# Optimization experiments

Hardware: AMD Instinct MI355X
Metric: run time of the kernel (lower is better)

## Reference

```python
import jax, jax.numpy as jnp
import numpy as np

QMIN, QMAX = 0.0, 255.0  # uint8 activation quantization range


def _qlinear(x, w_q, b, s_in, zp_in, s_w):
    """zentorch_qlinear: quantize fp32 x to uint8, int8 weight, dequant output.

    x:   [M, K] fp32
    w_q: [N, K] int8 values (stored int32), symmetric (weight zp = 0)
    b:   [N] fp32
    s_in, zp_in: scalars (activation scale / zero point)
    s_w: [N] per-output-channel weight scales
    """
    zp = zp_in.astype(jnp.float32)
    q = jnp.clip(jnp.round(x / s_in) + zp, QMIN, QMAX)      # fake-quant uint8
    x_dq = (q - zp) * s_in                                   # dequantized activation
    w_dq = w_q.astype(jnp.float32) * s_w[:, None]            # [N, K] dequant weight
    return x_dq @ w_dq.T + b                                 # [M, N] fp32


def setup_inputs() -> dict:
    key = jax.random.key(0)
    k1, k2, k3, k4 = jax.random.split(key, 4)
    M, K, N = 8192, 4096, 4096
    inp = {
        "input": jax.random.normal(k1, (M, K), dtype=jnp.float32),
        "weights": jax.random.randint(k2, (N, K), -128, 128, dtype=jnp.int32),
        "biases": jax.random.normal(k3, (N,), dtype=jnp.float32) * 0.1,
        "input_scales": jnp.array([0.05], dtype=jnp.float32),
        "input_zero_points": jnp.array([128], dtype=jnp.int32),
        "weight_scales": jax.random.uniform(k4, (N,), dtype=jnp.float32, minval=0.001, maxval=0.01),
        "weight_zero_points": jnp.zeros((N,), dtype=jnp.int32),
        "output_dtype": 0,  # 0 -> float32
    }
    return inp


def reference(input, weights, biases, input_scales, input_zero_points,
              weight_scales, weight_zero_points, output_dtype):
    s_in = input_scales[0]
    zp_in = input_zero_points[0]
    x = _qlinear(input, weights, biases, s_in, zp_in, weight_scales)
    x = _qlinear(x, weights, biases, s_in, zp_in, weight_scales)
    x = _qlinear(x, weights, biases, s_in, zp_in, weight_scales)
    return x
```

## Files before the change

kernel.cpp:

```cpp
#include <hip/hip_runtime.h>
#include <stdint.h>

#define M_DIM 8192
#define K_DIM 4096
#define N_DIM 4096
#define KTILES (K_DIM / 64)

typedef __attribute__((ext_vector_type(4))) int i32x4;

__global__ void pack_w_kernel(const int* __restrict__ w, char* __restrict__ wp,
                              int* __restrict__ corr, const int* __restrict__ zpp) {
  __shared__ int red[256];
  const int n = blockIdx.x;
  const int t = threadIdx.x;
  const int kt = t >> 2;
  const int g = t & 3;
  const int* row = w + (size_t)n * K_DIM + kt * 64 + g * 16;
  int s = 0;
  int words[4];
#pragma unroll
  for (int u = 0; u < 4; ++u) {
    int4 v = *(const int4*)(row + u * 4);
    s += v.x + v.y + v.z + v.w;
    words[u] = (v.x & 255) | ((v.y & 255) << 8) | ((v.z & 255) << 16) | (v.w << 24);
  }
  const int b = n & ~63;
  const int idx = n & 63;
  const int j = idx & 3;
  const int r = idx >> 2;
  const int F = (b >> 4) + j;
  char* dst = wp + ((size_t)F * 64 + kt) * 1024 + (g * 16 + r) * 16;
  *(int4*)dst = make_int4(words[0], words[1], words[2], words[3]);
  red[t] = s;
  __syncthreads();
  for (int off = 128; off > 0; off >>= 1) {
    if (t < off) red[t] += red[t + off];
    __syncthreads();
  }
  if (t == 0) corr[n] = (128 - zpp[0]) * red[0];
}

__global__ void quant_in_kernel(const float* __restrict__ x, char* __restrict__ q,
                                const float* __restrict__ sp, const int* __restrict__ zpp) {
  const int i = blockIdx.x * blockDim.x + threadIdx.x;
  const float s = sp[0];
  const float zp = (float)zpp[0];
  float4 v = ((const float4*)x)[i];
  float t0 = fminf(fmaxf(rintf(v.x / s) + zp, 0.f), 255.f);
  float t1 = fminf(fmaxf(rintf(v.y / s) + zp, 0.f), 255.f);
  float t2 = fminf(fmaxf(rintf(v.z / s) + zp, 0.f), 255.f);
  float t3 = fminf(fmaxf(rintf(v.w / s) + zp, 0.f), 255.f);
  int b0 = (int)t0 - 128, b1 = (int)t1 - 128, b2 = (int)t2 - 128, b3 = (int)t3 - 128;
  ((int*)q)[i] = (b0 & 255) | ((b1 & 255) << 8) | ((b2 & 255) << 16) | (b3 << 24);
}

#define STAGE16(SRC, DST)                                                     \
  __builtin_amdgcn_global_load_lds(                                           \
      (const __attribute__((address_space(1))) void*)(SRC),                   \
      (__attribute__((address_space(3))) void*)(DST), 16, 0, 0)

#define RD(p) (*(const i32x4*)(p))

#define TILE(SLOT, KSTG, TN, DO_NEXT)                                         \
  {                                                                           \
    const char* bufA_ = &lds[SLOT][0];                                        \
    char* nA_ = &lds[((SLOT) + 3) & 3][0];                                    \
    i32x4 a1_[4];                                                             \
    _Pragma("unroll") for (int i_ = 0; i_ < 4; ++i_)                          \
        a1_[i_] = RD(bufA_ + aoff[4 + i_]);                                   \
    STAGE16(asrc0 + (size_t)(KSTG) * 64, nA_ + o0_);                          \
    STAGE16(asrc1 + (size_t)(KSTG) * 64, nA_ + o1_);                          \
    __builtin_amdgcn_s_setprio(1);                                            \
    _Pragma("unroll") for (int i_ = 0; i_ < 4; ++i_)                          \
        _Pragma("unroll") for (int j_ = 0; j_ < 4; ++j_)                      \
            acc[i_][j_] = __builtin_amdgcn_mfma_i32_16x16x64_i8(              \
                a0[i_], b0[j_], acc[i_][j_], 0, 0, 0);                        \
    __builtin_amdgcn_s_setprio(0);                                            \
    i32x4 ta_[4], bn_[4];                                                     \
    if (DO_NEXT) {                                                            \
      const char* xA_ = &lds[((SLOT) + 1) & 3][0];                            \
      _Pragma("unroll") for (int i_ = 0; i_ < 4; ++i_)                        \
          ta_[i_] = RD(xA_ + aoff[i_]);                                       \
      _Pragma("unroll") for (int j_ = 0; j_ < 4; ++j_)                        \
          bn_[j_] = RD(bptr[j_] + (size_t)(TN) * 1024);                       \
    }                                                                         \
    __builtin_amdgcn_s_setprio(1);                                            \
    _Pragma("unroll") for (int i_ = 0; i_ < 4; ++i_)                          \
        _Pragma("unroll") for (int j_ = 0; j_ < 4; ++j_)                      \
            acc[4 + i_][j_] = __builtin_amdgcn_mfma_i32_16x16x64_i8(          \
                a1_[i_], b0[j_], acc[4 + i_][j_], 0, 0, 0);                   \
    __builtin_amdgcn_s_setprio(0);                                            \
    asm volatile("s_waitcnt vmcnt(12)" ::: "memory");                         \
    __builtin_amdgcn_s_barrier();                                             \
    if (DO_NEXT) {                                                            \
      _Pragma("unroll") for (int i_ = 0; i_ < 4; ++i_) a0[i_] = ta_[i_];      \
      _Pragma("unroll") for (int j_ = 0; j_ < 4; ++j_) b0[j_] = bn_[j_];      \
    }                                                                         \
  }

template <int WRITE_Q>
__global__ __launch_bounds__(512, 2) void gemm_kernel(
    const char* __restrict__ qa, const char* __restrict__ wbp,
    const int* __restrict__ corr, const float* __restrict__ swp,
    const float* __restrict__ bias, const float* __restrict__ sp,
    const int* __restrict__ zpp, char* __restrict__ outq, float* __restrict__ outf) {
  __shared__ __align__(16) char lds[4][16384];
  const int tid = threadIdx.x;
  const int lane = tid & 63;
  const int w = tid >> 6;
  const int wr = w >> 2;
  const int wc = w & 3;
  const int bid = blockIdx.x;
  const int bm = bid & 31;
  const int bn = bid >> 5;
  const char* abase = qa + (size_t)bm * 256 * K_DIM;

  const int o0_ = tid * 16;
  const int o1_ = 8192 + tid * 16;
  const int r0_ = o0_ >> 6, r1_ = o1_ >> 6;
  const int g0_ = ((o0_ >> 4) & 3) ^ ((r0_ >> 1) & 3);
  const int g1_ = ((o1_ >> 4) & 3) ^ ((r1_ >> 1) & 3);
  const char* asrc0 = abase + (size_t)r0_ * K_DIM + g0_ * 16;
  const char* asrc1 = abase + (size_t)r1_ * K_DIM + g1_ * 16;

  const int Fbase = (bn * 256 + wc * 64) >> 4;
  const char* bptr[4];
#pragma unroll
  for (int j = 0; j < 4; ++j)
    bptr[j] = wbp + (size_t)(Fbase + j) * 64 * 1024 + lane * 16;

  const int rr = lane & 15;
  const int g = lane >> 4;
  int aoff[8];
#pragma unroll
  for (int i = 0; i < 8; ++i) {
    const int row = wr * 128 + i * 16 + rr;
    aoff[i] = (row << 6) + ((g ^ ((row >> 1) & 3)) << 4);
  }

  i32x4 acc[8][4] = {};

  STAGE16(asrc0, &lds[0][o0_]); STAGE16(asrc1, &lds[0][o1_]);
  STAGE16(asrc0 + 64, &lds[1][o0_]); STAGE16(asrc1 + 64, &lds[1][o1_]);
  STAGE16(asrc0 + 128, &lds[2][o0_]); STAGE16(asrc1 + 128, &lds[2][o1_]);
  i32x4 a0[4], b0[4];
#pragma unroll
  for (int j = 0; j < 4; ++j) b0[j] = RD(bptr[j]);
  asm volatile("s_waitcnt vmcnt(8)" ::: "memory");
  __builtin_amdgcn_s_barrier();
#pragma unroll
  for (int i = 0; i < 4; ++i) a0[i] = RD(&lds[0][0] + aoff[i]);

  for (int tb = 0; tb < (KTILES - 4) / 4; ++tb) {
    const int t0 = tb * 4;
#pragma unroll
    for (int u = 0; u < 4; ++u) {
      TILE(u, t0 + u + 3, t0 + u + 1, 1);
    }
  }
  TILE(0, KTILES - 1, 61, 1);
  TILE(1, KTILES - 1, 62, 1);
  TILE(2, KTILES - 1, 63, 1);
  TILE(3, KTILES - 1, 63, 0);
  asm volatile("s_waitcnt vmcnt(0)" ::: "memory");

  const float s = sp[0];
  const float zpf = (float)zpp[0];
  const int m0 = bm * 256 + wr * 128 + (lane >> 4) * 4;
  const int nb4 = bn * 256 + wc * 64 + ((lane & 15) << 2);
  const int4 cr4 = *(const int4*)(corr + nb4);
  const float4 sw4 = *(const float4*)(swp + nb4);
  const float4 bb4 = *(const float4*)(bias + nb4);
  const float fs0 = s * sw4.x, fs1 = s * sw4.y, fs2 = s * sw4.z, fs3 = s * sw4.w;
#pragma unroll
  for (int i = 0; i < 8; ++i) {
#pragma unroll
    for (int q = 0; q < 4; ++q) {
      const int m = m0 + i * 16 + q;
      const float v0 = fs0 * (float)(acc[i][0][q] + cr4.x) + bb4.x;
      const float v1 = fs1 * (float)(acc[i][1][q] + cr4.y) + bb4.y;
      const float v2 = fs2 * (float)(acc[i][2][q] + cr4.z) + bb4.z;
      const float v3 = fs3 * (float)(acc[i][3][q] + cr4.w) + bb4.w;
      if (WRITE_Q) {
        const int b0i = (int)fminf(fmaxf(rintf(v0 / s) + zpf, 0.f), 255.f) - 128;
        const int b1i = (int)fminf(fmaxf(rintf(v1 / s) + zpf, 0.f), 255.f) - 128;
        const int b2i = (int)fminf(fmaxf(rintf(v2 / s) + zpf, 0.f), 255.f) - 128;
        const int b3i = (int)fminf(fmaxf(rintf(v3 / s) + zpf, 0.f), 255.f) - 128;
        const uint32_t pk = (uint32_t)(b0i & 255) | ((uint32_t)(b1i & 255) << 8) |
                            ((uint32_t)(b2i & 255) << 16) | ((uint32_t)b3i << 24);
        *(uint32_t*)(outq + (size_t)m * N_DIM + nb4) = pk;
      } else {
        float4 o4;
        o4.x = v0; o4.y = v1; o4.z = v2; o4.w = v3;
        *(float4*)(outf + (size_t)m * N_DIM + nb4) = o4;
      }
    }
  }
}

extern "C" void kernel_launch(void* const* d_in, const int* in_sizes, int n_in,
                              void* d_out, int out_size, void* d_ws, size_t ws_size,
                              hipStream_t stream) {
  const float* x = (const float*)d_in[0];
  const int* wq = (const int*)d_in[1];
  const float* bias = (const float*)d_in[2];
  const float* s_in = (const float*)d_in[3];
  const int* zp_in = (const int*)d_in[4];
  const float* s_w = (const float*)d_in[5];
  float* out = (float*)d_out;

  const size_t WP_BYTES = (size_t)N_DIM * K_DIM;
  const size_t Q_BYTES = (size_t)M_DIM * K_DIM;
  char* ws = (char*)d_ws;
  char* wp = ws;
  char* q1 = ws + WP_BYTES;
  char* q2 = q1 + Q_BYTES;
  int* corr = (int*)(q2 + Q_BYTES);
  const size_t NEEDED = WP_BYTES + 2 * Q_BYTES + (size_t)N_DIM * sizeof(int);
  if (ws_size < NEEDED) return;

  pack_w_kernel<<<N_DIM, 256, 0, stream>>>(wq, wp, corr, zp_in);
  quant_in_kernel<<<(M_DIM * K_DIM / 4) / 256, 256, 0, stream>>>(x, q1, s_in, zp_in);

  dim3 grid((M_DIM / 256) * (N_DIM / 256));
  dim3 blk(512);
  gemm_kernel<1><<<grid, blk, 0, stream>>>(q1, wp, corr, s_w, bias, s_in, zp_in, q2, nullptr);
  gemm_kernel<1><<<grid, blk, 0, stream>>>(q2, wp, corr, s_w, bias, s_in, zp_in, q1, nullptr);
  gemm_kernel<0><<<grid, blk, 0, stream>>>(q1, wp, corr, s_w, bias, s_in, zp_in, nullptr, out);
}
```

Baseline: 450.5 us.

## Pre-pack activations into MFMA fragment layout and drop LDS staging in GEMM

```diff
diff --git a/kernel.cpp b/kernel.cpp
--- a/kernel.cpp
+++ b/kernel.cpp
@@ -24,12 +24,9 @@
     s += v.x + v.y + v.z + v.w;
     words[u] = (v.x & 255) | ((v.y & 255) << 8) | ((v.z & 255) << 16) | (v.w << 24);
   }
-  const int b = n & ~63;
-  const int idx = n & 63;
-  const int j = idx & 3;
-  const int r = idx >> 2;
-  const int F = (b >> 4) + j;
-  char* dst = wp + ((size_t)F * 64 + kt) * 1024 + (g * 16 + r) * 16;
+  const int j = n & 3;
+  const int r = (n & 63) >> 2;
+  char* dst = wp + ((size_t)(n >> 6) * 64 + kt) * 4096 + j * 1024 + (g * 16 + r) * 16;
   *(int4*)dst = make_int4(words[0], words[1], words[2], words[3]);
   red[t] = s;
   __syncthreads();
@@ -42,60 +39,55 @@
 
 __global__ void quant_in_kernel(const float* __restrict__ x, char* __restrict__ q,
                                 const float* __restrict__ sp, const int* __restrict__ zpp) {
-  const int i = blockIdx.x * blockDim.x + threadIdx.x;
+  const int b = blockIdx.x;
+  const int t = threadIdx.x;
   const float s = sp[0];
   const float zp = (float)zpp[0];
-  float4 v = ((const float4*)x)[i];
-  float t0 = fminf(fmaxf(rintf(v.x / s) + zp, 0.f), 255.f);
-  float t1 = fminf(fmaxf(rintf(v.y / s) + zp, 0.f), 255.f);
-  float t2 = fminf(fmaxf(rintf(v.z / s) + zp, 0.f), 255.f);
-  float t3 = fminf(fmaxf(rintf(v.w / s) + zp, 0.f), 255.f);
-  int b0 = (int)t0 - 128, b1 = (int)t1 - 128, b2 = (int)t2 - 128, b3 = (int)t3 - 128;
-  ((int*)q)[i] = (b0 & 255) | ((b1 & 255) << 8) | ((b2 & 255) << 16) | (b3 << 24);
+  const int slot = t & 63;
+  const int g4 = slot >> 4;
+  const int r = slot & 15;
+  const float* src0 = x + (size_t)(16 * b + r) * K_DIM + g4 * 16;
+  char* dst0 = q + (size_t)(b >> 3) * 524288 + (b & 7) * 1024 + slot * 16;
+#pragma unroll 4
+  for (int u = 0; u < 16; ++u) {
+    const int kt = u * 4 + (t >> 6);
+    const float4* src = (const float4*)(src0 + kt * 64);
+    int words[4];
+#pragma unroll
+    for (int v4 = 0; v4 < 4; ++v4) {
+      float4 v = src[v4];
+      int b0 = (int)fminf(fmaxf(rintf(v.x / s) + zp, 0.f), 255.f) - 128;
+      int b1 = (int)fminf(fmaxf(rintf(v.y / s) + zp, 0.f), 255.f) - 128;
+      int b2 = (int)fminf(fmaxf(rintf(v.z / s) + zp, 0.f), 255.f) - 128;
+      int b3 = (int)fminf(fmaxf(rintf(v.w / s) + zp, 0.f), 255.f) - 128;
+      words[v4] = (b0 & 255) | ((b1 & 255) << 8) | ((b2 & 255) << 16) | (b3 << 24);
+    }
+    *(int4*)(dst0 + (size_t)kt * 8192) = make_int4(words[0], words[1], words[2], words[3]);
+  }
 }
-
-#define STAGE16(SRC, DST)                                                     \
-  __builtin_amdgcn_global_load_lds(                                           \
-      (const __attribute__((address_space(1))) void*)(SRC),                   \
-      (__attribute__((address_space(3))) void*)(DST), 16, 0, 0)
 
 #define RD(p) (*(const i32x4*)(p))
 
-#define TILE(SLOT, KSTG, TN, DO_NEXT)                                         \
+#define BODY(TNEXT, CA, CB, NA, NB, DO_NEXT)                                  \
   {                                                                           \
-    const char* bufA_ = &lds[SLOT][0];                                        \
-    char* nA_ = &lds[((SLOT) + 3) & 3][0];                                    \
-    i32x4 a1_[4];                                                             \
-    _Pragma("unroll") for (int i_ = 0; i_ < 4; ++i_)                          \
-        a1_[i_] = RD(bufA_ + aoff[4 + i_]);                                   \
-    STAGE16(asrc0 + (size_t)(KSTG) * 64, nA_ + o0_);                          \
-    STAGE16(asrc1 + (size_t)(KSTG) * 64, nA_ + o1_);                          \
+    if (DO_NEXT) {                                                            \
+      const char* aT_ = abase + (size_t)(TNEXT) * 8192;                       \
+      const char* bT_ = bbase + (size_t)(TNEXT) * 4096;                       \
+      _Pragma("unroll") for (int i_ = 0; i_ < 8; ++i_)                        \
+          NA[i_] = RD(aT_ + i_ * 1024);                                       \
+      _Pragma("unroll") for (int j_ = 0; j_ < 4; ++j_)                        \
+          NB[j_] = RD(bT_ + j_ * 1024);                                       \
+      asm volatile("s_waitcnt vmcnt(12)" ::: "memory");                       \
+    } else {                                                                  \
+      asm volatile("s_waitcnt vmcnt(0)" ::: "memory");                        \
+    }                                                                         \
+    __builtin_amdgcn_s_barrier();                                             \
     __builtin_amdgcn_s_setprio(1);                                            \
-    _Pragma("unroll") for (int i_ = 0; i_ < 4; ++i_)                          \
+    _Pragma("unroll") for (int i_ = 0; i_ < 8; ++i_)                          \
         _Pragma("unroll") for (int j_ = 0; j_ < 4; ++j_)                      \
             acc[i_][j_] = __builtin_amdgcn_mfma_i32_16x16x64_i8(              \
-                a0[i_], b0[j_], acc[i_][j_], 0, 0, 0);                        \
+                CA[i_], CB[j_], acc[i_][j_], 0, 0, 0);                        \
     __builtin_amdgcn_s_setprio(0);                                            \
-    i32x4 ta_[4], bn_[4];                                                     \
-    if (DO_NEXT) {                                                            \
-      const char* xA_ = &lds[((SLOT) + 1) & 3][0];                            \
-      _Pragma("unroll") for (int i_ = 0; i_ < 4; ++i_)                        \
-          ta_[i_] = RD(xA_ + aoff[i_]);                                       \
-      _Pragma("unroll") for (int j_ = 0; j_ < 4; ++j_)                        \
-          bn_[j_] = RD(bptr[j_] + (size_t)(TN) * 1024);                       \
-    }                                                                         \
-    __builtin_amdgcn_s_setprio(1);                                            \
-    _Pragma("unroll") for (int i_ = 0; i_ < 4; ++i_)                          \
-        _Pragma("unroll") for (int j_ = 0; j_ < 4; ++j_)                      \
-            acc[4 + i_][j_] = __builtin_amdgcn_mfma_i32_16x16x64_i8(          \
-                a1_[i_], b0[j_], acc[4 + i_][j_], 0, 0, 0);                   \
-    __builtin_amdgcn_s_setprio(0);                                            \
-    asm volatile("s_waitcnt vmcnt(12)" ::: "memory");                         \
-    __builtin_amdgcn_s_barrier();                                             \
-    if (DO_NEXT) {                                                            \
-      _Pragma("unroll") for (int i_ = 0; i_ < 4; ++i_) a0[i_] = ta_[i_];      \
-      _Pragma("unroll") for (int j_ = 0; j_ < 4; ++j_) b0[j_] = bn_[j_];      \
-    }                                                                         \
   }
 
 template <int WRITE_Q>
@@ -104,7 +96,6 @@
     const int* __restrict__ corr, const float* __restrict__ swp,
     const float* __restrict__ bias, const float* __restrict__ sp,
     const int* __restrict__ zpp, char* __restrict__ outq, float* __restrict__ outf) {
-  __shared__ __align__(16) char lds[4][16384];
   const int tid = threadIdx.x;
   const int lane = tid & 63;
   const int w = tid >> 6;
@@ -113,65 +104,39 @@
   const int bid = blockIdx.x;
   const int bm = bid & 31;
   const int bn = bid >> 5;
-  const char* abase = qa + (size_t)bm * 256 * K_DIM;
 
-  const int o0_ = tid * 16;
-  const int o1_ = 8192 + tid * 16;
-  const int r0_ = o0_ >> 6, r1_ = o1_ >> 6;
-  const int g0_ = ((o0_ >> 4) & 3) ^ ((r0_ >> 1) & 3);
-  const int g1_ = ((o1_ >> 4) & 3) ^ ((r1_ >> 1) & 3);
-  const char* asrc0 = abase + (size_t)r0_ * K_DIM + g0_ * 16;
-  const char* asrc1 = abase + (size_t)r1_ * K_DIM + g1_ * 16;
-
-  const int Fbase = (bn * 256 + wc * 64) >> 4;
-  const char* bptr[4];
-#pragma unroll
-  for (int j = 0; j < 4; ++j)
-    bptr[j] = wbp + (size_t)(Fbase + j) * 64 * 1024 + lane * 16;
-
-  const int rr = lane & 15;
-  const int g = lane >> 4;
-  int aoff[8];
-#pragma unroll
-  for (int i = 0; i < 8; ++i) {
-    const int row = wr * 128 + i * 16 + rr;
-    aoff[i] = (row << 6) + ((g ^ ((row >> 1) & 3)) << 4);
-  }
+  const char* abase = qa + (size_t)(bm * 2 + wr) * 524288 + lane * 16;
+  const char* bbase = wbp + (size_t)(bn * 4 + wc) * 262144 + lane * 16;
 
   i32x4 acc[8][4] = {};
+  i32x4 ca[8], cb[4], na[8], nb[4];
 
-  STAGE16(asrc0, &lds[0][o0_]); STAGE16(asrc1, &lds[0][o1_]);
-  STAGE16(asrc0 + 64, &lds[1][o0_]); STAGE16(asrc1 + 64, &lds[1][o1_]);
-  STAGE16(asrc0 + 128, &lds[2][o0_]); STAGE16(asrc1 + 128, &lds[2][o1_]);
-  i32x4 a0[4], b0[4];
 #pragma unroll
-  for (int j = 0; j < 4; ++j) b0[j] = RD(bptr[j]);
-  asm volatile("s_waitcnt vmcnt(8)" ::: "memory");
-  __builtin_amdgcn_s_barrier();
+  for (int i = 0; i < 8; ++i) ca[i] = RD(abase + i * 1024);
 #pragma unroll
-  for (int i = 0; i < 4; ++i) a0[i] = RD(&lds[0][0] + aoff[i]);
+  for (int j = 0; j < 4; ++j) cb[j] = RD(bbase + j * 1024);
 
-  for (int tb = 0; tb < (KTILES - 4) / 4; ++tb) {
-    const int t0 = tb * 4;
-#pragma unroll
-    for (int u = 0; u < 4; ++u) {
-      TILE(u, t0 + u + 3, t0 + u + 1, 1);
-    }
+  for (int t = 0; t < KTILES - 2; t += 2) {
+    BODY(t + 1, ca, cb, na, nb, 1)
+    BODY(t + 2, na, nb, ca, cb, 1)
   }
-  TILE(0, KTILES - 1, 61, 1);
-  TILE(1, KTILES - 1, 62, 1);
-  TILE(2, KTILES - 1, 63, 1);
-  TILE(3, KTILES - 1, 63, 0);
-  asm volatile("s_waitcnt vmcnt(0)" ::: "memory");
+  BODY(KTILES - 1, ca, cb, na, nb, 1)
+  BODY(0, na, nb, ca, cb, 0)
 
   const float s = sp[0];
   const float zpf = (float)zpp[0];
-  const int m0 = bm * 256 + wr * 128 + (lane >> 4) * 4;
-  const int nb4 = bn * 256 + wc * 64 + ((lane & 15) << 2);
+  const int c = lane & 15;
+  const int qg = lane >> 4;
+  const int m0 = bm * 256 + wr * 128 + qg * 4;
+  const int nb4 = bn * 256 + wc * 64 + (c << 2);
   const int4 cr4 = *(const int4*)(corr + nb4);
   const float4 sw4 = *(const float4*)(swp + nb4);
   const float4 bb4 = *(const float4*)(bias + nb4);
   const float fs0 = s * sw4.x, fs1 = s * sw4.y, fs2 = s * sw4.z, fs3 = s * sw4.w;
+  char* qdst = outq
+                   ? outq + ((size_t)(bm * 2 + wr) * 64 + bn * 4 + wc) * 8192 +
+                         ((c >> 2) * 16) * 16 + 4 * (c & 3)
+                   : nullptr;
 #pragma unroll
   for (int i = 0; i < 8; ++i) {
 #pragma unroll
@@ -188,7 +153,7 @@
         const int b3i = (int)fminf(fmaxf(rintf(v3 / s) + zpf, 0.f), 255.f) - 128;
         const uint32_t pk = (uint32_t)(b0i & 255) | ((uint32_t)(b1i & 255) << 8) |
                             ((uint32_t)(b2i & 255) << 16) | ((uint32_t)b3i << 24);
-        *(uint32_t*)(outq + (size_t)m * N_DIM + nb4) = pk;
+        *(uint32_t*)(qdst + i * 1024 + (qg * 4 + q) * 16) = pk;
       } else {
         float4 o4;
         o4.x = v0; o4.y = v1; o4.z = v2; o4.w = v3;
@@ -220,7 +185,7 @@
   if (ws_size < NEEDED) return;
 
   pack_w_kernel<<<N_DIM, 256, 0, stream>>>(wq, wp, corr, zp_in);
-  quant_in_kernel<<<(M_DIM * K_DIM / 4) / 256, 256, 0, stream>>>(x, q1, s_in, zp_in);
+  quant_in_kernel<<<M_DIM / 16, 256, 0, stream>>>(x, q1, s_in, zp_in);
 
   dim3 grid((M_DIM / 256) * (N_DIM / 256));
   dim3 blk(512);
```

Result: slower. 466.7 us (+3.6%).
